# Kernel optimization log

Hardware: AMD Instinct MI355X
Metric: run time of the kernel (lower is better)

## Reference

```python
import jax, jax.numpy as jnp
import numpy as np

N, E = 50000, 400000          # nodes, edges
IN, H, OUT = 256, 512, 256    # channels
L, K = 2, 2                   # num_layers, Chebyshev order


def setup_inputs() -> dict:
    key = jax.random.key(0)
    ks = jax.random.split(key, 8)
    x = jax.random.normal(ks[0], (N, IN), jnp.float32)
    edge_index = jax.random.randint(ks[1], (2, E), 0, N)
    in_w = jax.random.normal(ks[2], (IN, H), jnp.float32) / np.float32(np.sqrt(IN))
    in_b = jnp.zeros((H,), jnp.float32)
    # ChebConv has K bias-free Linear layers per conv plus one bias vector
    conv_w = jax.random.normal(ks[3], (L, K, H, H), jnp.float32) / np.float32(np.sqrt(H))
    conv_b = jnp.zeros((L, H), jnp.float32)
    out_w = jax.random.normal(ks[4], (H, OUT), jnp.float32) / np.float32(np.sqrt(H))
    out_b = jnp.zeros((OUT,), jnp.float32)
    return dict(x=x, edge_index=edge_index, in_w=in_w, in_b=in_b,
                conv_w=conv_w, conv_b=conv_b, out_w=out_w, out_b=out_b)


def reference(x, edge_index, in_w, in_b, conv_w, conv_b, out_w, out_b):
    # PyG ChebConv normalization with lambda_max=2 (default):
    #   L_hat = 2/lambda_max * (I - D^{-1/2} A D^{-1/2}) - I = -D^{-1/2} A D^{-1/2}
    # i.e. off-diagonal weights -dinv[row]*w*dinv[col], diagonal 0.
    row, col = edge_index[0], edge_index[1]
    w = jnp.ones((E,), x.dtype)
    deg = jax.ops.segment_sum(w, row, num_segments=N)
    dinv = jnp.where(deg > 0, jax.lax.rsqrt(jnp.maximum(deg, 1e-12)), 0.0).astype(x.dtype)
    norm = -dinv[row] * w * dinv[col]  # [E]

    def prop(h):  # L_hat @ h  (gather from source row, scatter-add to target col)
        return jax.ops.segment_sum(norm[:, None] * h[row], col, num_segments=N)

    # dropout is identity in eval mode; reference is deterministic (eval)
    h = jax.nn.silu(x @ in_w + in_b)
    for l in range(L):
        # Chebyshev recursion, K=2: out = Tx0 @ W0 + (L_hat Tx0) @ W1 + b
        Tx0 = h
        out = Tx0 @ conv_w[l, 0]
        Tx1 = prop(Tx0)
        out = out + Tx1 @ conv_w[l, 1] + conv_b[l]
        h = jax.nn.silu(out)
    return h @ out_w + out_b
```

## Files before the change

kernel.cpp:

```cpp
#include <hip/hip_runtime.h>

#define H512 512

typedef short bf16x8 __attribute__((ext_vector_type(8)));
typedef float f32x4  __attribute__((ext_vector_type(4)));

__device__ __forceinline__ float silu_f(float v) { return v / (1.0f + __expf(-v)); }

__device__ __forceinline__ short f2bf(float f) {
    unsigned u = __float_as_uint(f);
    u = (u + 0x7FFFu + ((u >> 16) & 1u)) >> 16;
    return (short)u;
}
__device__ __forceinline__ float bf2f(short s) {
    return __uint_as_float(((unsigned)(unsigned short)s) << 16);
}

__device__ __forceinline__ int xcd_swz(int b, int nwg) {
    const int NX = 8;
    int q = nwg / NX, rr = nwg % NX;
    int xcd = b % NX, idx = b / NX;
    int base = (xcd < rr) ? xcd * (q + 1) : rr * (q + 1) + (xcd - rr) * q;
    return base + idx;
}


__global__ void hist_kernel(const int* __restrict__ row, const int* __restrict__ col,
                            float* __restrict__ deg, int* __restrict__ cnt, int E) {
    int e = blockIdx.x * blockDim.x + threadIdx.x;
    if (e < E) {
        atomicAdd(&deg[row[e]], 1.0f);
        atomicAdd(&cnt[col[e]], 1);
    }
}

__global__ void dinv_kernel(const float* __restrict__ deg, float* __restrict__ dinv, int n) {
    int i = blockIdx.x * blockDim.x + threadIdx.x;
    if (i < n) {
        float d = deg[i];
        dinv[i] = d > 0.0f ? rsqrtf(fmaxf(d, 1e-12f)) : 0.0f;
    }
}


__global__ __launch_bounds__(256) void bsum_kernel(const int* __restrict__ cnt,
                                                   int* __restrict__ bsum, int n) {
    __shared__ int s[4];
    int i = blockIdx.x * 256 + threadIdx.x;
    int v = (i < n) ? cnt[i] : 0;
    #pragma unroll
    for (int off = 32; off; off >>= 1) v += __shfl_down(v, off, 64);
    if ((threadIdx.x & 63) == 0) s[threadIdx.x >> 6] = v;
    __syncthreads();
    if (threadIdx.x == 0) bsum[blockIdx.x] = s[0] + s[1] + s[2] + s[3];
}

__global__ __launch_bounds__(256) void bscan_kernel(const int* __restrict__ bsum,
                                                    int* __restrict__ boff, int B) {
    __shared__ int s[256];
    int tid = threadIdx.x;
    int v = (tid < B) ? bsum[tid] : 0;
    s[tid] = v;
    __syncthreads();
    #pragma unroll
    for (int off = 1; off < 256; off <<= 1) {
        int t = (tid >= off) ? s[tid - off] : 0;
        __syncthreads();
        s[tid] += t;
        __syncthreads();
    }
    if (tid < B) boff[tid] = s[tid] - v;
}

__global__ __launch_bounds__(256) void cscan_kernel(const int* __restrict__ cnt,
                                                    const int* __restrict__ boff,
                                                    int* __restrict__ ptr,
                                                    int* __restrict__ ptr2, int n, int B) {
    __shared__ int s[256];
    int b = blockIdx.x, tid = threadIdx.x;
    int i = b * 256 + tid;
    int v = (i < n) ? cnt[i] : 0;
    s[tid] = v;
    __syncthreads();
    #pragma unroll
    for (int off = 1; off < 256; off <<= 1) {
        int t = (tid >= off) ? s[tid - off] : 0;
        __syncthreads();
        s[tid] += t;
        __syncthreads();
    }
    int exc = boff[b] + s[tid] - v;
    if (i < n) { ptr[i] = exc; ptr2[i] = exc; }
    if (b == B - 1 && tid == 255) ptr[n] = exc + v;
}

__global__ void scatter_kernel(const int* __restrict__ row, const int* __restrict__ col,
                               const float* __restrict__ dinv, int* __restrict__ ptr2,
                               int* __restrict__ esrc, float* __restrict__ ew, int E) {
    int e = blockIdx.x * blockDim.x + threadIdx.x;
    if (e >= E) return;
    int r = row[e], c = col[e];
    int pos = atomicAdd(&ptr2[c], 1);
    esrc[pos] = r;
    ew[pos]   = -dinv[r] * dinv[c];
}


__global__ __launch_bounds__(256) void wt_kernel(const float* __restrict__ W,
                                                 short* __restrict__ Wt, int K, int Nw) {
    __shared__ float tile[32][33];
    const int tx = threadIdx.x & 31;
    const int ty = threadIdx.x >> 5;
    const int nt = Nw / 32;
    const int k0 = (blockIdx.x / nt) * 32;
    const int n0 = (blockIdx.x % nt) * 32;
    #pragma unroll
    for (int i = 0; i < 4; ++i) {
        const int k = ty + i * 8;
        tile[k][tx] = W[(size_t)(k0 + k) * Nw + n0 + tx];
    }
    __syncthreads();
    #pragma unroll
    for (int i = 0; i < 4; ++i) {
        const int a = ty + i * 8;
        Wt[(size_t)(n0 + a) * K + k0 + tx] = f2bf(tile[tx][a]);
    }
}

__global__ void xconv_kernel(const float* __restrict__ x, short* __restrict__ xb,
                             int Nreal, int Mpad) {
    int tid = blockIdx.x * blockDim.x + threadIdx.x;
    if (tid >= Mpad * 32) return;
    int r = tid >> 5, c8 = (tid & 31) * 8;
    bf16x8 o = {0, 0, 0, 0, 0, 0, 0, 0};
    if (r < Nreal) {
        const float4 f0 = *(const float4*)(x + (size_t)r * 256 + c8);
        const float4 f1 = *(const float4*)(x + (size_t)r * 256 + c8 + 4);
        o[0] = f2bf(f0.x); o[1] = f2bf(f0.y); o[2] = f2bf(f0.z); o[3] = f2bf(f0.w);
        o[4] = f2bf(f1.x); o[5] = f2bf(f1.y); o[6] = f2bf(f1.z); o[7] = f2bf(f1.w);
    }
    *(bf16x8*)(xb + (size_t)r * 256 + c8) = o;
}


__global__ __launch_bounds__(256) void gather_kernel(
    const int* __restrict__ ptr, const int* __restrict__ esrc,
    const float* __restrict__ ew, const short* __restrict__ T,
    short* __restrict__ U, int N_)
{
    int t = threadIdx.x;
    int node = blockIdx.x * 4 + (t >> 6);
    if (node >= N_) return;
    int q = (t & 63) * 8;
    float acc[8] = {0.f, 0.f, 0.f, 0.f, 0.f, 0.f, 0.f, 0.f};
    const int i1 = ptr[node + 1];
    for (int i = ptr[node]; i < i1; ++i) {
        int s   = esrc[i];
        float w = ew[i];
        bf16x8 tv = *(const bf16x8*)(T + (size_t)s * H512 + q);
        #pragma unroll
        for (int j = 0; j < 8; ++j) acc[j] += w * bf2f(tv[j]);
    }
    bf16x8 o;
    #pragma unroll
    for (int j = 0; j < 8; ++j) o[j] = f2bf(acc[j]);
    *(bf16x8*)(U + (size_t)node * H512 + q) = o;
}


template<int ACCUM, int BIAS, int SILU, int F32OUT>
__global__ __launch_bounds__(256) void mfma_gemm(
    const short* __restrict__ A, int lda,
    const short* __restrict__ Bt, int ldb,
    const short* __restrict__ Cin, void* __restrict__ Cout, int ldc,
    const float* __restrict__ bias, int Mreal, int K, int gx)
{
    __shared__ alignas(16) short lds[4 * 128 * 64];

    const int t    = threadIdx.x;
    const int lane = t & 63;
    const int wid  = t >> 6;

    const int wg = xcd_swz(blockIdx.x, gridDim.x);
    const int m0 = (wg / gx) * 128;
    const int n0 = (wg % gx) * 128;

    const int wm = wid >> 1;
    const int wn = wid & 1;

    const int srow  = lane >> 3;
    const int scol  = (lane & 7) * 16;
    const int corig = scol ^ (srow << 4);
    const int cel   = corig >> 1;

    f32x4 acc[4][4];
    #pragma unroll
    for (int m = 0; m < 4; ++m)
        #pragma unroll
        for (int n = 0; n < 4; ++n)
            acc[m][n] = (f32x4){0.f, 0.f, 0.f, 0.f};

    const int r = lane & 15;
    const int g = lane >> 4;

    auto stage = [&](int buf, int k0) {
        short* Ad = lds + buf * 16384;
        short* Bd = Ad + 8192;
        #pragma unroll
        for (int i = 0; i < 4; ++i) {
            const int r0 = (wid * 4 + i) * 8;
            const short* ga = A + (size_t)(m0 + r0 + srow) * lda + (k0 + cel);
            __builtin_amdgcn_global_load_lds(
                (const __attribute__((address_space(1))) void*)ga,
                (__attribute__((address_space(3))) void*)(Ad + r0 * 64), 16, 0, 0);
            const short* gb = Bt + (size_t)(n0 + r0 + srow) * ldb + (k0 + cel);
            __builtin_amdgcn_global_load_lds(
                (const __attribute__((address_space(1))) void*)gb,
                (__attribute__((address_space(3))) void*)(Bd + r0 * 64), 16, 0, 0);
        }
    };

    const int nt = K >> 6;
    stage(0, 0);
    stage(1, 64);

    for (int tt = 0; tt < nt; ++tt) {
        if (tt + 1 < nt) asm volatile("s_waitcnt vmcnt(8)" ::: "memory");
        else             asm volatile("s_waitcnt vmcnt(0)" ::: "memory");
        __builtin_amdgcn_s_barrier();
        asm volatile("" ::: "memory");

        const short* Ab = lds + (tt & 1) * 16384;
        const short* Bb = Ab + 8192;

        #pragma unroll
        for (int ks = 0; ks < 2; ++ks) {
            bf16x8 af[4], bfr[4];
            #pragma unroll
            for (int m = 0; m < 4; ++m) {
                const int rowA = wm * 64 + m * 16 + r;
                const int cb   = (ks * 64 + g * 16) ^ ((rowA & 7) << 4);
                af[m] = *(const bf16x8*)((const char*)Ab + rowA * 128 + cb);
            }
            #pragma unroll
            for (int n = 0; n < 4; ++n) {
                const int rowB = wn * 64 + n * 16 + r;
                const int cb   = (ks * 64 + g * 16) ^ ((rowB & 7) << 4);
                bfr[n] = *(const bf16x8*)((const char*)Bb + rowB * 128 + cb);
            }
            #pragma unroll
            for (int m = 0; m < 4; ++m)
                #pragma unroll
                for (int n = 0; n < 4; ++n)
                    acc[m][n] = __builtin_amdgcn_mfma_f32_16x16x32_bf16(
                        af[m], bfr[n], acc[m][n], 0, 0, 0);
        }

        asm volatile("" ::: "memory");
        __builtin_amdgcn_s_barrier();
        asm volatile("" ::: "memory");
        if (tt + 2 < nt) stage(tt & 1, (tt + 2) * 64);
    }

    __syncthreads();
    float* fs = (float*)lds;
    #pragma unroll
    for (int m = 0; m < 4; ++m) {
        #pragma unroll
        for (int j = 0; j < 4; ++j) {
            const int row = wm * 64 + m * 16 + g * 4 + j;
            const int rot = (row & 15) << 2;
            #pragma unroll
            for (int n = 0; n < 4; ++n) {
                const int cl = (n * 16 + r + rot) & 63;
                fs[row * 128 + wn * 64 + cl] = acc[m][n][j];
            }
        }
    }
    __syncthreads();

    const int rrow = t >> 1;
    const int hf   = t & 1;
    const int gr   = m0 + rrow;
    const int rot2 = (rrow & 15) << 2;

    float vv[64];
    #pragma unroll
    for (int c4 = 0; c4 < 16; ++c4) {
        const int cl = (c4 * 4 + rot2) & 63;
        *(f32x4*)&vv[c4 * 4] = *(const f32x4*)&fs[rrow * 128 + hf * 64 + cl];
    }
    const int gc0 = n0 + hf * 64;
    if (ACCUM) {
        #pragma unroll
        for (int c8 = 0; c8 < 8; ++c8) {
            bf16x8 ci = *(const bf16x8*)(Cin + (size_t)gr * ldc + gc0 + c8 * 8);
            #pragma unroll
            for (int j = 0; j < 8; ++j) vv[c8 * 8 + j] += bf2f(ci[j]);
        }
    }
    if (BIAS) {
        #pragma unroll
        for (int c4 = 0; c4 < 16; ++c4) {
            const float4 bv = *(const float4*)(bias + gc0 + c4 * 4);
            vv[c4 * 4 + 0] += bv.x; vv[c4 * 4 + 1] += bv.y;
            vv[c4 * 4 + 2] += bv.z; vv[c4 * 4 + 3] += bv.w;
        }
    }
    if (SILU) {
        #pragma unroll
        for (int j = 0; j < 64; ++j) vv[j] = silu_f(vv[j]);
    }
    if (F32OUT) {
        if (gr < Mreal) {
            #pragma unroll
            for (int c4 = 0; c4 < 16; ++c4)
                *(float4*)((float*)Cout + (size_t)gr * ldc + gc0 + c4 * 4) =
                    make_float4(vv[c4*4+0], vv[c4*4+1], vv[c4*4+2], vv[c4*4+3]);
        }
    } else {
        #pragma unroll
        for (int c8 = 0; c8 < 8; ++c8) {
            bf16x8 o;
            #pragma unroll
            for (int j = 0; j < 8; ++j) o[j] = f2bf(vv[c8 * 8 + j]);
            *(bf16x8*)((short*)Cout + (size_t)gr * ldc + gc0 + c8 * 8) = o;
        }
    }
}


extern "C" void kernel_launch(void* const* d_in, const int* in_sizes, int n_in,
                              void* d_out, int out_size, void* d_ws, size_t ws_size,
                              hipStream_t stream)
{
    const float* x      = (const float*)d_in[0];
    const int*   ei     = (const int*)  d_in[1];
    const float* in_w   = (const float*)d_in[2];
    const float* in_b   = (const float*)d_in[3];
    const float* conv_w = (const float*)d_in[4];
    const float* conv_b = (const float*)d_in[5];
    const float* out_w  = (const float*)d_in[6];
    const float* out_b  = (const float*)d_in[7];

    const int N = in_sizes[0] / 256;
    const int E = in_sizes[1] / 2;
    const int MPAD = ((N + 127) / 128) * 128;
    const int* row = ei;
    const int* col = ei + E;

    char* p = (char*)d_ws;
    short* h0 = (short*)p; p += (size_t)MPAD * H512 * 2;
    short* h1 = (short*)p; p += (size_t)MPAD * H512 * 2;
    short* T  = (short*)p; p += (size_t)MPAD * H512 * 2;
    short* U  = (short*)p; p += (size_t)MPAD * H512 * 2;
    short* xb = T;
    short* wti = (short*)p; p += (size_t)512 * 256 * 2;
    short* wtc = (short*)p; p += (size_t)4 * 512 * 512 * 2;
    short* wto = (short*)p; p += (size_t)256 * 512 * 2;
    float* deg  = (float*)p; p += (size_t)N * 4;
    float* dinv = (float*)p; p += (size_t)N * 4;
    float* ew   = (float*)p; p += (size_t)E * 4;
    int*   cnt  = (int*)p;   p += (size_t)N * 4;
    int*   ptr  = (int*)p;   p += (size_t)(N + 4) * 4;
    int*   ptr2 = (int*)p;   p += (size_t)N * 4;
    int*   esrc = (int*)p;   p += (size_t)E * 4;
    int*   bsum = (int*)p;   p += (size_t)256 * 4;
    int*   boff = (int*)p;   p += (size_t)256 * 4;

    const int NB = (N + 255) / 256;

    hipMemsetAsync(deg, 0, (size_t)N * sizeof(float), stream);
    hipMemsetAsync(cnt, 0, (size_t)N * sizeof(int), stream);
    hist_kernel<<<(E + 255) / 256, 256, 0, stream>>>(row, col, deg, cnt, E);
    dinv_kernel<<<(N + 255) / 256, 256, 0, stream>>>(deg, dinv, N);
    bsum_kernel <<<NB, 256, 0, stream>>>(cnt, bsum, N);
    bscan_kernel<<<1, 256, 0, stream>>>(bsum, boff, NB);
    cscan_kernel<<<NB, 256, 0, stream>>>(cnt, boff, ptr, ptr2, N, NB);
    scatter_kernel<<<(E + 255) / 256, 256, 0, stream>>>(row, col, dinv, ptr2, esrc, ew, E);

    wt_kernel<<<(256 / 32) * (512 / 32), 256, 0, stream>>>(in_w, wti, 256, 512);
    for (int i = 0; i < 4; ++i)
        wt_kernel<<<(512 / 32) * (512 / 32), 256, 0, stream>>>(
            conv_w + (size_t)i * 512 * 512, wtc + (size_t)i * 512 * 512, 512, 512);
    wt_kernel<<<(512 / 32) * (256 / 32), 256, 0, stream>>>(out_w, wto, 512, 256);
    xconv_kernel<<<(MPAD * 32 + 255) / 256, 256, 0, stream>>>(x, xb, N, MPAD);

    const int mt = MPAD / 128;

    mfma_gemm<0, 1, 1, 0><<<dim3(4 * mt), 256, 0, stream>>>(
        xb, 256, wti, 256, nullptr, h0, H512, in_b, N, 256, 4);

    short* hc = h0;
    short* hn = h1;
    for (int l = 0; l < 2; ++l) {
        mfma_gemm<0, 0, 0, 0><<<dim3(4 * mt), 256, 0, stream>>>(
            hc, H512, wtc + (size_t)(l * 2 + 1) * 512 * 512, 512,
            nullptr, T, H512, nullptr, N, 512, 4);
        gather_kernel<<<(N + 3) / 4, 256, 0, stream>>>(ptr, esrc, ew, T, U, N);
        mfma_gemm<1, 1, 1, 0><<<dim3(4 * mt), 256, 0, stream>>>(
            hc, H512, wtc + (size_t)(l * 2 + 0) * 512 * 512, 512,
            U, hn, H512, conv_b + (size_t)l * H512, N, 512, 4);
        short* tmp = hc; hc = hn; hn = tmp;
    }

    mfma_gemm<0, 1, 0, 1><<<dim3(2 * mt), 256, 0, stream>>>(
        hc, H512, wto, 512, nullptr, d_out, 256, out_b, N, 512, 2);
}
```

Baseline: 534.5 us.

## Propagate before projecting and fuse conv GEMMs into one concatenated-K GEMM

Result: slower. 613.7 us (+14.8%).

```diff
diff --git a/kernel.cpp b/kernel.cpp
--- a/kernel.cpp
+++ b/kernel.cpp
@@ -41,7 +41,6 @@
         dinv[i] = d > 0.0f ? rsqrtf(fmaxf(d, 1e-12f)) : 0.0f;
     }
 }
-
 
 __global__ __launch_bounds__(256) void bsum_kernel(const int* __restrict__ cnt,
                                                    int* __restrict__ bsum, int n) {
@@ -107,7 +106,8 @@
 
 
 __global__ __launch_bounds__(256) void wt_kernel(const float* __restrict__ W,
-                                                 short* __restrict__ Wt, int K, int Nw) {
+                                                 short* __restrict__ Wt, int K, int Nw,
+                                                 int ldWt, int koff) {
     __shared__ float tile[32][33];
     const int tx = threadIdx.x & 31;
     const int ty = threadIdx.x >> 5;
@@ -123,7 +123,7 @@
     #pragma unroll
     for (int i = 0; i < 4; ++i) {
         const int a = ty + i * 8;
-        Wt[(size_t)(n0 + a) * K + k0 + tx] = f2bf(tile[tx][a]);
+        Wt[(size_t)(n0 + a) * ldWt + koff + k0 + tx] = f2bf(tile[tx][a]);
     }
 }
 
@@ -146,12 +146,17 @@
 __global__ __launch_bounds__(256) void gather_kernel(
     const int* __restrict__ ptr, const int* __restrict__ esrc,
     const float* __restrict__ ew, const short* __restrict__ T,
-    short* __restrict__ U, int N_)
+    short* __restrict__ U, int Nreal, int Mpad)
 {
     int t = threadIdx.x;
     int node = blockIdx.x * 4 + (t >> 6);
-    if (node >= N_) return;
+    if (node >= Mpad) return;
     int q = (t & 63) * 8;
+    if (node >= Nreal) {
+        bf16x8 z = {0, 0, 0, 0, 0, 0, 0, 0};
+        *(bf16x8*)(U + (size_t)node * H512 + q) = z;
+        return;
+    }
     float acc[8] = {0.f, 0.f, 0.f, 0.f, 0.f, 0.f, 0.f, 0.f};
     const int i1 = ptr[node + 1];
     for (int i = ptr[node]; i < i1; ++i) {
@@ -168,14 +173,14 @@
 }
 
 
-template<int ACCUM, int BIAS, int SILU, int F32OUT>
+template<int SILU, int F32OUT>
 __global__ __launch_bounds__(256) void mfma_gemm(
-    const short* __restrict__ A, int lda,
+    const short* __restrict__ A0, const short* __restrict__ A1, int ksplit, int lda,
     const short* __restrict__ Bt, int ldb,
-    const short* __restrict__ Cin, void* __restrict__ Cout, int ldc,
+    void* __restrict__ Cout, int ldc,
     const float* __restrict__ bias, int Mreal, int K, int gx)
 {
-    __shared__ alignas(16) short lds[4 * 128 * 64];
+    __shared__ alignas(16) short As[2][128 * 64];
 
     const int t    = threadIdx.x;
     const int lane = t & 63;
@@ -193,6 +198,9 @@
     const int corig = scol ^ (srow << 4);
     const int cel   = corig >> 1;
 
+    const int r = lane & 15;
+    const int g = lane >> 4;
+
     f32x4 acc[4][4];
     #pragma unroll
     for (int m = 0; m < 4; ++m)
@@ -200,42 +208,35 @@
         for (int n = 0; n < 4; ++n)
             acc[m][n] = (f32x4){0.f, 0.f, 0.f, 0.f};
 
-    const int r = lane & 15;
-    const int g = lane >> 4;
-
-    auto stage = [&](int buf, int k0) {
-        short* Ad = lds + buf * 16384;
-        short* Bd = Ad + 8192;
+    const int nt = K >> 6;
+
+    auto stageA = [&](int buf, int kt) {
+        const int k0 = kt * 64;
+        const short* Abase = (k0 < ksplit) ? (A0 + k0) : (A1 + (k0 - ksplit));
         #pragma unroll
         for (int i = 0; i < 4; ++i) {
             const int r0 = (wid * 4 + i) * 8;
-            const short* ga = A + (size_t)(m0 + r0 + srow) * lda + (k0 + cel);
+            const short* ga = Abase + (size_t)(m0 + r0 + srow) * lda + cel;
             __builtin_amdgcn_global_load_lds(
                 (const __attribute__((address_space(1))) void*)ga,
-                (__attribute__((address_space(3))) void*)(Ad + r0 * 64), 16, 0, 0);
-            const short* gb = Bt + (size_t)(n0 + r0 + srow) * ldb + (k0 + cel);
-            __builtin_amdgcn_global_load_lds(
-                (const __attribute__((address_space(1))) void*)gb,
-                (__attribute__((address_space(3))) void*)(Bd + r0 * 64), 16, 0, 0);
+                (__attribute__((address_space(3))) void*)(As[buf] + r0 * 64), 16, 0, 0);
         }
     };
-
-    const int nt = K >> 6;
-    stage(0, 0);
-    stage(1, 64);
-
-    for (int tt = 0; tt < nt; ++tt) {
-        if (tt + 1 < nt) asm volatile("s_waitcnt vmcnt(8)" ::: "memory");
-        else             asm volatile("s_waitcnt vmcnt(0)" ::: "memory");
-        __builtin_amdgcn_s_barrier();
-        asm volatile("" ::: "memory");
-
-        const short* Ab = lds + (tt & 1) * 16384;
-        const short* Bb = Ab + 8192;
-
+    auto loadB = [&](bf16x8* bb, int kt) {
+        const int kb = kt * 64;
+        #pragma unroll
+        for (int ks = 0; ks < 2; ++ks)
+            #pragma unroll
+            for (int n = 0; n < 4; ++n) {
+                const int rowB = n0 + wn * 64 + n * 16 + r;
+                bb[ks * 4 + n] = *(const bf16x8*)(Bt + (size_t)rowB * ldb + kb + ks * 32 + g * 8);
+            }
+    };
+    auto mmstep = [&](int cur, const bf16x8* bb) {
+        const short* Ab = As[cur];
         #pragma unroll
         for (int ks = 0; ks < 2; ++ks) {
-            bf16x8 af[4], bfr[4];
+            bf16x8 af[4];
             #pragma unroll
             for (int m = 0; m < 4; ++m) {
                 const int rowA = wm * 64 + m * 16 + r;
@@ -243,88 +244,86 @@
                 af[m] = *(const bf16x8*)((const char*)Ab + rowA * 128 + cb);
             }
             #pragma unroll
-            for (int n = 0; n < 4; ++n) {
-                const int rowB = wn * 64 + n * 16 + r;
-                const int cb   = (ks * 64 + g * 16) ^ ((rowB & 7) << 4);
-                bfr[n] = *(const bf16x8*)((const char*)Bb + rowB * 128 + cb);
-            }
-            #pragma unroll
             for (int m = 0; m < 4; ++m)
                 #pragma unroll
                 for (int n = 0; n < 4; ++n)
                     acc[m][n] = __builtin_amdgcn_mfma_f32_16x16x32_bf16(
-                        af[m], bfr[n], acc[m][n], 0, 0, 0);
+                        af[m], bb[ks * 4 + n], acc[m][n], 0, 0, 0);
         }
-
-        asm volatile("" ::: "memory");
+    };
+
+    bf16x8 b0[8], b1[8];
+    stageA(0, 0);
+    loadB(b0, 0);
+    __builtin_amdgcn_sched_barrier(0);
+    stageA(1, 1);
+    __builtin_amdgcn_sched_barrier(0);
+
+    for (int tt = 0; tt < nt; tt += 2) {
+        asm volatile("s_waitcnt vmcnt(12)" ::: "memory");
         __builtin_amdgcn_s_barrier();
-        asm volatile("" ::: "memory");
-        if (tt + 2 < nt) stage(tt & 1, (tt + 2) * 64);
-    }
-
-    __syncthreads();
-    float* fs = (float*)lds;
-    #pragma unroll
-    for (int m = 0; m < 4; ++m) {
-        #pragma unroll
-        for (int j = 0; j < 4; ++j) {
-            const int row = wm * 64 + m * 16 + g * 4 + j;
-            const int rot = (row & 15) << 2;
+        __builtin_amdgcn_sched_barrier(0);
+        loadB(b1, (tt + 1 < nt) ? tt + 1 : nt - 1);
+        mmstep(0, b0);
+        __builtin_amdgcn_sched_barrier(0);
+        __builtin_amdgcn_s_barrier();
+        if (tt + 2 < nt) stageA(0, tt + 2);
+        asm volatile("s_waitcnt vmcnt(12)" ::: "memory");
+        __builtin_amdgcn_s_barrier();
+        __builtin_amdgcn_sched_barrier(0);
+        loadB(b0, (tt + 2 < nt) ? tt + 2 : nt - 1);
+        mmstep(1, b1);
+        __builtin_amdgcn_sched_barrier(0);
+        __builtin_amdgcn_s_barrier();
+        if (tt + 3 < nt) stageA(1, tt + 3);
+    }
+
+    float bb[4];
+    #pragma unroll
+    for (int n = 0; n < 4; ++n) bb[n] = bias[n0 + wn * 64 + n * 16 + r];
+
+    if (F32OUT) {
+        #pragma unroll
+        for (int m = 0; m < 4; ++m)
             #pragma unroll
-            for (int n = 0; n < 4; ++n) {
-                const int cl = (n * 16 + r + rot) & 63;
-                fs[row * 128 + wn * 64 + cl] = acc[m][n][j];
+            for (int j = 0; j < 4; ++j) {
+                const int rr = m0 + wm * 64 + m * 16 + g * 4 + j;
+                #pragma unroll
+                for (int n = 0; n < 4; ++n) {
+                    float v = acc[m][n][j] + bb[n];
+                    if (SILU) v = silu_f(v);
+                    if (rr < Mreal)
+                        ((float*)Cout)[(size_t)rr * ldc + n0 + wn * 64 + n * 16 + r] = v;
+                }
             }
-        }
-    }
-    __syncthreads();
-
-    const int rrow = t >> 1;
-    const int hf   = t & 1;
-    const int gr   = m0 + rrow;
-    const int rot2 = (rrow & 15) << 2;
-
-    float vv[64];
-    #pragma unroll
-    for (int c4 = 0; c4 < 16; ++c4) {
-        const int cl = (c4 * 4 + rot2) & 63;
-        *(f32x4*)&vv[c4 * 4] = *(const f32x4*)&fs[rrow * 128 + hf * 64 + cl];
-    }
-    const int gc0 = n0 + hf * 64;
-    if (ACCUM) {
+    } else {
+        __syncthreads();
+        short* fs = (short*)As;
+        #pragma unroll
+        for (int m = 0; m < 4; ++m)
+            #pragma unroll
+            for (int j = 0; j < 4; ++j) {
+                const int row = wm * 64 + m * 16 + g * 4 + j;
+                const int rot = (row & 15) << 3;
+                #pragma unroll
+                for (int n = 0; n < 4; ++n) {
+                    float v = acc[m][n][j] + bb[n];
+                    if (SILU) v = silu_f(v);
+                    const int col = wn * 64 + n * 16 + r;
+                    fs[row * 128 + ((col + rot) & 127)] = f2bf(v);
+                }
+            }
+        __syncthreads();
+        const int rr   = t >> 1;
+        const int hf   = t & 1;
+        const int rot2 = (rr & 15) << 3;
+        const size_t gr = (size_t)(m0 + rr);
         #pragma unroll
         for (int c8 = 0; c8 < 8; ++c8) {
-            bf16x8 ci = *(const bf16x8*)(Cin + (size_t)gr * ldc + gc0 + c8 * 8);
-            #pragma unroll
-            for (int j = 0; j < 8; ++j) vv[c8 * 8 + j] += bf2f(ci[j]);
-        }
-    }
-    if (BIAS) {
-        #pragma unroll
-        for (int c4 = 0; c4 < 16; ++c4) {
-            const float4 bv = *(const float4*)(bias + gc0 + c4 * 4);
-            vv[c4 * 4 + 0] += bv.x; vv[c4 * 4 + 1] += bv.y;
-            vv[c4 * 4 + 2] += bv.z; vv[c4 * 4 + 3] += bv.w;
-        }
-    }
-    if (SILU) {
-        #pragma unroll
-        for (int j = 0; j < 64; ++j) vv[j] = silu_f(vv[j]);
-    }
-    if (F32OUT) {
-        if (gr < Mreal) {
-            #pragma unroll
-            for (int c4 = 0; c4 < 16; ++c4)
-                *(float4*)((float*)Cout + (size_t)gr * ldc + gc0 + c4 * 4) =
-                    make_float4(vv[c4*4+0], vv[c4*4+1], vv[c4*4+2], vv[c4*4+3]);
-        }
-    } else {
-        #pragma unroll
-        for (int c8 = 0; c8 < 8; ++c8) {
-            bf16x8 o;
-            #pragma unroll
-            for (int j = 0; j < 8; ++j) o[j] = f2bf(vv[c8 * 8 + j]);
-            *(bf16x8*)((short*)Cout + (size_t)gr * ldc + gc0 + c8 * 8) = o;
+            const int cbase = hf * 64 + c8 * 8;
+            const int cl    = (cbase + rot2) & 127;
+            bf16x8 v8 = *(const bf16x8*)&fs[rr * 128 + cl];
+            *(bf16x8*)((short*)Cout + gr * ldc + n0 + cbase) = v8;
         }
     }
 }
@@ -352,11 +351,10 @@
     char* p = (char*)d_ws;
     short* h0 = (short*)p; p += (size_t)MPAD * H512 * 2;
     short* h1 = (short*)p; p += (size_t)MPAD * H512 * 2;
-    short* T  = (short*)p; p += (size_t)MPAD * H512 * 2;
-    short* U  = (short*)p; p += (size_t)MPAD * H512 * 2;
-    short* xb = T;
+    short* G  = (short*)p; p += (size_t)MPAD * H512 * 2;
+    short* xb = G;
     short* wti = (short*)p; p += (size_t)512 * 256 * 2;
-    short* wtc = (short*)p; p += (size_t)4 * 512 * 512 * 2;
+    short* wf  = (short*)p; p += (size_t)2 * 512 * 1024 * 2;
     short* wto = (short*)p; p += (size_t)256 * 512 * 2;
     float* deg  = (float*)p; p += (size_t)N * 4;
     float* dinv = (float*)p; p += (size_t)N * 4;
@@ -379,31 +377,30 @@
     cscan_kernel<<<NB, 256, 0, stream>>>(cnt, boff, ptr, ptr2, N, NB);
     scatter_kernel<<<(E + 255) / 256, 256, 0, stream>>>(row, col, dinv, ptr2, esrc, ew, E);
 
-    wt_kernel<<<(256 / 32) * (512 / 32), 256, 0, stream>>>(in_w, wti, 256, 512);
-    for (int i = 0; i < 4; ++i)
-        wt_kernel<<<(512 / 32) * (512 / 32), 256, 0, stream>>>(
-            conv_w + (size_t)i * 512 * 512, wtc + (size_t)i * 512 * 512, 512, 512);
-    wt_kernel<<<(512 / 32) * (256 / 32), 256, 0, stream>>>(out_w, wto, 512, 256);
+    wt_kernel<<<(256 / 32) * (512 / 32), 256, 0, stream>>>(in_w, wti, 256, 512, 256, 0);
+    for (int l = 0; l < 2; ++l)
+        for (int j = 0; j < 2; ++j)
+            wt_kernel<<<(512 / 32) * (512 / 32), 256, 0, stream>>>(
+                conv_w + (size_t)(l * 2 + j) * 512 * 512,
+                wf + (size_t)l * 512 * 1024, 512, 512, 1024, j * 512);
+    wt_kernel<<<(512 / 32) * (256 / 32), 256, 0, stream>>>(out_w, wto, 512, 256, 512, 0);
     xconv_kernel<<<(MPAD * 32 + 255) / 256, 256, 0, stream>>>(x, xb, N, MPAD);
 
     const int mt = MPAD / 128;
 
-    mfma_gemm<0, 1, 1, 0><<<dim3(4 * mt), 256, 0, stream>>>(
-        xb, 256, wti, 256, nullptr, h0, H512, in_b, N, 256, 4);
+    mfma_gemm<1, 0><<<dim3(4 * mt), 256, 0, stream>>>(
+        xb, xb, 256, 256, wti, 256, h0, H512, in_b, N, 256, 4);
 
     short* hc = h0;
     short* hn = h1;
     for (int l = 0; l < 2; ++l) {
-        mfma_gemm<0, 0, 0, 0><<<dim3(4 * mt), 256, 0, stream>>>(
-            hc, H512, wtc + (size_t)(l * 2 + 1) * 512 * 512, 512,
-            nullptr, T, H512, nullptr, N, 512, 4);
-        gather_kernel<<<(N + 3) / 4, 256, 0, stream>>>(ptr, esrc, ew, T, U, N);
-        mfma_gemm<1, 1, 1, 0><<<dim3(4 * mt), 256, 0, stream>>>(
-            hc, H512, wtc + (size_t)(l * 2 + 0) * 512 * 512, 512,
-            U, hn, H512, conv_b + (size_t)l * H512, N, 512, 4);
+        gather_kernel<<<(MPAD + 3) / 4, 256, 0, stream>>>(ptr, esrc, ew, hc, G, N, MPAD);
+        mfma_gemm<1, 0><<<dim3(4 * mt), 256, 0, stream>>>(
+            hc, G, 512, H512, wf + (size_t)l * 512 * 1024, 1024,
+            hn, H512, conv_b + (size_t)l * H512, N, 1024, 4);
         short* tmp = hc; hc = hn; hn = tmp;
     }
 
-    mfma_gemm<0, 1, 0, 1><<<dim3(2 * mt), 256, 0, stream>>>(
-        hc, H512, wto, 512, nullptr, d_out, 256, out_b, N, 512, 2);
-}
+    mfma_gemm<0, 1><<<dim3(2 * mt), 256, 0, stream>>>(
+        hc, hc, 512, H512, wto, 512, d_out, 256, out_b, N, 512, 2);
+}
```
